# Kernel tuning notes

Measured on AMD Instinct MI355X. Metric: run time of the kernel, lower is better.

## Reference

```python
import jax, jax.numpy as jnp
import numpy as np

D = 1024
H = 16
HD = D // H  # 64


def setup_inputs() -> dict:
    key = jax.random.key(0)
    ks = jax.random.split(key, 12)
    B, S = 2, 2048
    inp = {
        "input_query": jax.random.normal(ks[0], (B, S, D), jnp.float32),
        "input_key": jax.random.normal(ks[1], (B, S, D), jnp.float32),
        "input_value": jax.random.normal(ks[2], (B, S, D), jnp.float32),
        "mask": jnp.ones((S, S), dtype=bool),  # ignored, as in original
        # per-head Q/K/V linears, stacked over heads: [H, D, HD]
        "Wq": jax.random.normal(ks[3], (H, D, HD), jnp.float32) / np.sqrt(D),
        "bq": jax.random.normal(ks[4], (H, HD), jnp.float32) * 0.01,
        "Wk": jax.random.normal(ks[5], (H, D, HD), jnp.float32) / np.sqrt(D),
        "bk": jax.random.normal(ks[6], (H, HD), jnp.float32) * 0.01,
        "Wv": jax.random.normal(ks[7], (H, D, HD), jnp.float32) / np.sqrt(D),
        "bv": jax.random.normal(ks[8], (H, HD), jnp.float32) * 0.01,
        "Wo": jax.random.normal(ks[9], (D, D), jnp.float32) / np.sqrt(D),
        "bo": jax.random.normal(ks[10], (D,), jnp.float32) * 0.01,
    }
    return inp


def reference(input_query, input_key, input_value, mask, Wq, bq, Wk, bk, Wv, bv, Wo, bo):
    B, S, _ = input_query.shape
    # batched per-head projections: [B,S,D] x [H,D,HD] -> [B,H,S,HD]
    q = jnp.einsum("bsd,hdk->bhsk", input_query, Wq) + bq[None, :, None, :]
    k = jnp.einsum("bsd,hdk->bhsk", input_key, Wk) + bk[None, :, None, :]
    v = jnp.einsum("bsd,hdk->bhsk", input_value, Wv) + bv[None, :, None, :]
    scale = 1.0 / np.sqrt(HD)
    scores = jnp.einsum("bhqk,bhsk->bhqs", q, k) * scale  # [B,H,S,S]
    causal = jnp.tril(jnp.ones((S, S), dtype=bool))
    scores = jnp.where(causal[None, None], scores, jnp.finfo(scores.dtype).min)
    p = jax.nn.softmax(scores, axis=-1)
    out = jnp.einsum("bhqs,bhsk->bhqk", p, v)  # [B,H,S,HD]
    # concat heads (matches torch.cat over head outputs on last dim)
    out = out.transpose(0, 2, 1, 3).reshape(B, S, D)
    return out @ Wo + bo
```

## Files before the change

kernel.cpp:

```cpp
#include <hip/hip_runtime.h>
#include <hip/hip_bf16.h>

typedef __bf16 bf16;
typedef bf16 bf16x8 __attribute__((ext_vector_type(8)));
typedef bf16 bf16x4 __attribute__((ext_vector_type(4)));
typedef float f32x4 __attribute__((ext_vector_type(4)));

#define B_  2
#define S_  2048
#define D_  1024
#define H_  16
#define HD_ 64
#define M_  4096
#define K_  1024
#define N_  1024

#if __has_builtin(__builtin_amdgcn_exp2f)
#define EXP2F(x) __builtin_amdgcn_exp2f(x)
#else
#define EXP2F(x) exp2f(x)
#endif

__device__ __forceinline__ void gld16(const bf16* g, bf16* l) {
    __builtin_amdgcn_global_load_lds(
        (const __attribute__((address_space(1))) unsigned int*)(g),
        (__attribute__((address_space(3))) unsigned int*)(l), 16, 0, 0);
}


__global__ void pack_x(const float* __restrict__ xq, const float* __restrict__ xk,
                       const float* __restrict__ xv, bf16* __restrict__ out) {
    int t = blockIdx.y;
    const float* src = (t == 0) ? xq : (t == 1) ? xk : xv;
    bf16* dst = out + (size_t)t * M_ * K_;
    int idx = (blockIdx.x * 256 + threadIdx.x) * 4;
    float4 v = *(const float4*)&src[idx];
    bf16x4 o = { (bf16)v.x, (bf16)v.y, (bf16)v.z, (bf16)v.w };
    *(bf16x4*)&dst[idx] = o;
}

__global__ void pack_w(const float* __restrict__ wq, const float* __restrict__ wk,
                       const float* __restrict__ wv, bf16* __restrict__ out) {
    int t = blockIdx.y;
    const float* src = (t == 0) ? wq : (t == 1) ? wk : wv;
    bf16* dst = out + (size_t)t * N_ * K_;
    int o = blockIdx.x * 256 + threadIdx.x;
    int n = o >> 10, k = o & 1023;
    dst[o] = (bf16)src[(n >> 6) * (D_ * HD_) + k * HD_ + (n & 63)];
}

__global__ void pack_wo(const float* __restrict__ wo, bf16* __restrict__ dst) {
    int o = blockIdx.x * 256 + threadIdx.x;
    int n = o >> 10, k = o & 1023;
    dst[o] = (bf16)wo[k * D_ + n];
}

__global__ __launch_bounds__(256) void gemm_qkv(
        const bf16* __restrict__ X, const bf16* __restrict__ Wt,
        const float* __restrict__ bq, const float* __restrict__ bk,
        const float* __restrict__ bv, bf16* __restrict__ QKV) {
    __shared__ __align__(16) bf16 As[128 * 32];
    __shared__ __align__(16) bf16 Bs[128 * 32];
    int t = blockIdx.z;
    const bf16* A = X + (size_t)t * M_ * K_;
    const bf16* W = Wt + (size_t)t * N_ * K_;
    const float* bias = (t == 0) ? bq : (t == 1) ? bk : bv;
    int m0 = blockIdx.x * 128, n0 = blockIdx.y * 128;
    int tid = threadIdx.x;
    int w = tid >> 6, l = tid & 63, lr = l & 15, lg = l >> 4;
    int wr = (w >> 1) * 64, wc = (w & 1) * 64;
    int srow = (l >> 2), scol = (l & 3) * 8;
    f32x4 acc[4][4] = {};
    for (int k0 = 0; k0 < K_; k0 += 32) {
        #pragma unroll
        for (int c = 0; c < 2; c++) {
            int chunk = w * 2 + c;
            gld16(&A[(size_t)(m0 + chunk * 16 + srow) * K_ + k0 + scol], &As[chunk * 512]);
            gld16(&W[(size_t)(n0 + chunk * 16 + srow) * K_ + k0 + scol], &Bs[chunk * 512]);
        }
        __syncthreads();
        bf16x8 af[4], bfr[4];
        #pragma unroll
        for (int mi = 0; mi < 4; mi++) af[mi] = *(const bf16x8*)&As[(wr + mi * 16 + lr) * 32 + lg * 8];
        #pragma unroll
        for (int ni = 0; ni < 4; ni++) bfr[ni] = *(const bf16x8*)&Bs[(wc + ni * 16 + lr) * 32 + lg * 8];
        #pragma unroll
        for (int mi = 0; mi < 4; mi++)
            #pragma unroll
            for (int ni = 0; ni < 4; ni++)
                acc[mi][ni] = __builtin_amdgcn_mfma_f32_16x16x32_bf16(af[mi], bfr[ni], acc[mi][ni], 0, 0, 0);
        __syncthreads();
    }
    float qscale = (t == 0) ? 0.125f * 1.4426950408889634f : 1.0f;
    #pragma unroll
    for (int mi = 0; mi < 4; mi++)
        #pragma unroll
        for (int ni = 0; ni < 4; ni++)
            #pragma unroll
            for (int i = 0; i < 4; i++) {
                int m = m0 + wr + mi * 16 + lg * 4 + i;
                int n = n0 + wc + ni * 16 + lr;
                float v = (acc[mi][ni][i] + bias[n]) * qscale;
                int b = m >> 11, s = m & 2047, h = n >> 6, hd = n & 63;
                QKV[((((size_t)t * B_ + b) * H_ + h) * S_ + s) * HD_ + hd] = (bf16)v;
            }
}

__global__ __launch_bounds__(256) void gemm_out(
        const bf16* __restrict__ A, const bf16* __restrict__ Wt,
        const float* __restrict__ bo, float* __restrict__ out) {
    __shared__ __align__(16) bf16 As[128 * 32];
    __shared__ __align__(16) bf16 Bs[128 * 32];
    int m0 = blockIdx.x * 128, n0 = blockIdx.y * 128;
    int tid = threadIdx.x;
    int w = tid >> 6, l = tid & 63, lr = l & 15, lg = l >> 4;
    int wr = (w >> 1) * 64, wc = (w & 1) * 64;
    int srow = (l >> 2), scol = (l & 3) * 8;
    f32x4 acc[4][4] = {};
    for (int k0 = 0; k0 < K_; k0 += 32) {
        #pragma unroll
        for (int c = 0; c < 2; c++) {
            int chunk = w * 2 + c;
            gld16(&A[(size_t)(m0 + chunk * 16 + srow) * K_ + k0 + scol], &As[chunk * 512]);
            gld16(&Wt[(size_t)(n0 + chunk * 16 + srow) * K_ + k0 + scol], &Bs[chunk * 512]);
        }
        __syncthreads();
        bf16x8 af[4], bfr[4];
        #pragma unroll
        for (int mi = 0; mi < 4; mi++) af[mi] = *(const bf16x8*)&As[(wr + mi * 16 + lr) * 32 + lg * 8];
        #pragma unroll
        for (int ni = 0; ni < 4; ni++) bfr[ni] = *(const bf16x8*)&Bs[(wc + ni * 16 + lr) * 32 + lg * 8];
        #pragma unroll
        for (int mi = 0; mi < 4; mi++)
            #pragma unroll
            for (int ni = 0; ni < 4; ni++)
                acc[mi][ni] = __builtin_amdgcn_mfma_f32_16x16x32_bf16(af[mi], bfr[ni], acc[mi][ni], 0, 0, 0);
        __syncthreads();
    }
    #pragma unroll
    for (int mi = 0; mi < 4; mi++)
        #pragma unroll
        for (int ni = 0; ni < 4; ni++)
            #pragma unroll
            for (int i = 0; i < 4; i++) {
                int m = m0 + wr + mi * 16 + lg * 4 + i;
                int n = n0 + wc + ni * 16 + lr;
                out[(size_t)m * N_ + n] = acc[mi][ni][i] + bo[n];
            }
}

__global__ __launch_bounds__(256) void transpose_v(const bf16* __restrict__ V,
                                                   bf16* __restrict__ VT) {
    __shared__ __align__(16) bf16 Ls[64][64];
    int s0 = blockIdx.x * 64, bh = blockIdx.y;
    const bf16* src = V + (size_t)bh * S_ * HD_;
    bf16* dst = VT + (size_t)bh * HD_ * S_;
    int tid = threadIdx.x;
    #pragma unroll
    for (int c = tid; c < 512; c += 256) {
        int row = c >> 3, cg = (c & 7) * 8;
        int cgp = cg ^ (((row >> 3) & 3) << 4);
        *(bf16x8*)&Ls[row][cgp] = *(const bf16x8*)&src[(size_t)(s0 + row) * 64 + cg];
    }
    __syncthreads();
    #pragma unroll
    for (int c = tid; c < 512; c += 256) {
        int hd = c >> 3, sg = (c & 7) * 8;
        bf16x8 v;
        #pragma unroll
        for (int e = 0; e < 8; e++) {
            int row = sg + e;
            v[e] = Ls[row][hd ^ (((row >> 3) & 3) << 4)];
        }
        *(bf16x8*)&dst[(size_t)hd * S_ + s0 + sg] = v;
    }
}

__global__ __launch_bounds__(512) void attn(const bf16* __restrict__ QKV,
                                            const bf16* __restrict__ VT,
                                            bf16* __restrict__ AO) {
    __shared__ __align__(16) bf16 Ks[2][64][72];
    __shared__ __align__(16) bf16 Vts[2][64][72];
    __shared__ __align__(16) bf16 Ps[8][16][72];
    int bh = blockIdx.y;
    int qt = (bh & 16) ? blockIdx.x : (15 - blockIdx.x);
    int q0 = qt * 128;
    const bf16* Qp = QKV + (size_t)bh * S_ * HD_;
    const bf16* Kp = QKV + (size_t)(32 + bh) * S_ * HD_;
    const bf16* VTp = VT + (size_t)bh * HD_ * S_;
    int tid = threadIdx.x, w = tid >> 6, l = tid & 63, lr = l & 15, lg = l >> 4;
    int srow = tid >> 3, scg = (tid & 7) * 8;

    bf16x8 aq[2];
    #pragma unroll
    for (int ks = 0; ks < 2; ks++)
        aq[ks] = *(const bf16x8*)&Qp[(size_t)(q0 + w * 16 + lr) * 64 + ks * 32 + lg * 8];

    f32x4 o[4] = {};
    float lsum[4] = {};
    int jmax = 2 * qt + 1;

    *(bf16x8*)&Ks[0][srow][scg]  = *(const bf16x8*)&Kp[(size_t)srow * 64 + scg];
    *(bf16x8*)&Vts[0][srow][scg] = *(const bf16x8*)&VTp[(size_t)srow * S_ + scg];
    __syncthreads();

    for (int j = 0; j <= jmax; ++j) {
        int cur = j & 1;
        if (j < jmax) {
            int nxt = cur ^ 1;
            *(bf16x8*)&Ks[nxt][srow][scg]  = *(const bf16x8*)&Kp[(size_t)((j + 1) * 64 + srow) * 64 + scg];
            *(bf16x8*)&Vts[nxt][srow][scg] = *(const bf16x8*)&VTp[(size_t)srow * S_ + (j + 1) * 64 + scg];
        }

        f32x4 sc[4] = {};
        __builtin_amdgcn_s_setprio(1);
        #pragma unroll
        for (int ks = 0; ks < 2; ks++)
            #pragma unroll
            for (int ni = 0; ni < 4; ni++) {
                bf16x8 bk_ = *(const bf16x8*)&Ks[cur][ni * 16 + lr][ks * 32 + lg * 8];
                sc[ni] = __builtin_amdgcn_mfma_f32_16x16x32_bf16(aq[ks], bk_, sc[ni], 0, 0, 0);
            }
        __builtin_amdgcn_s_setprio(0);

        bool diag = (j >= 2 * qt);
        int qrow = w * 16 + lg * 4;
        int kvb = j * 64 - q0;
        #pragma unroll
        for (int ni = 0; ni < 4; ni++)
            #pragma unroll
            for (int i = 0; i < 4; i++) {
                float s = sc[ni][i];
                if (diag && (kvb + ni * 16 + lr > qrow + i)) s = -30000.0f;
                float p = EXP2F(s);
                lsum[i] += p;
                Ps[w][lg * 4 + i][ni * 16 + lr] = (bf16)p;
            }

        __builtin_amdgcn_s_setprio(1);
        #pragma unroll
        for (int ks = 0; ks < 2; ks++) {
            bf16x8 ap = *(const bf16x8*)&Ps[w][lr][ks * 32 + lg * 8];
            #pragma unroll
            for (int nf = 0; nf < 4; nf++) {
                bf16x8 bv_ = *(const bf16x8*)&Vts[cur][nf * 16 + lr][ks * 32 + lg * 8];
                o[nf] = __builtin_amdgcn_mfma_f32_16x16x32_bf16(ap, bv_, o[nf], 0, 0, 0);
            }
        }
        __builtin_amdgcn_s_setprio(0);
        __syncthreads();
    }

    #pragma unroll
    for (int i = 0; i < 4; i++) {
        #pragma unroll
        for (int xm = 1; xm < 16; xm <<= 1) lsum[i] += __shfl_xor(lsum[i], xm);
    }

    int b = bh >> 4, h = bh & 15;
    #pragma unroll
    for (int i = 0; i < 4; i++) {
        float inv = 1.0f / lsum[i];
        #pragma unroll
        for (int nf = 0; nf < 4; nf++) {
            int m = b * S_ + q0 + w * 16 + lg * 4 + i;
            int d = h * 64 + nf * 16 + lr;
            AO[(size_t)m * D_ + d] = (bf16)(o[nf][i] * inv);
        }
    }
}

extern "C" void kernel_launch(void* const* d_in, const int* in_sizes, int n_in,
                              void* d_out, int out_size, void* d_ws, size_t ws_size,
                              hipStream_t stream) {
    const float* xq = (const float*)d_in[0];
    const float* xk = (const float*)d_in[1];
    const float* xv = (const float*)d_in[2];
    const float* wq = (const float*)d_in[4];
    const float* bq = (const float*)d_in[5];
    const float* wk = (const float*)d_in[6];
    const float* bk = (const float*)d_in[7];
    const float* wv = (const float*)d_in[8];
    const float* bv = (const float*)d_in[9];
    const float* wo = (const float*)d_in[10];
    const float* bo = (const float*)d_in[11];
    float* out = (float*)d_out;

    bf16* Xb  = (bf16*)d_ws;
    bf16* Wb  = Xb  + (size_t)3 * M_ * K_;
    bf16* WoT = Wb  + (size_t)3 * N_ * K_;
    bf16* QKV = WoT + (size_t)N_ * K_;
    bf16* AO  = QKV + (size_t)3 * M_ * K_;
    bf16* VT  = Xb;

    pack_x <<<dim3(M_ * K_ / 1024, 3), 256, 0, stream>>>(xq, xk, xv, Xb);
    pack_w <<<dim3(N_ * K_ / 256, 3), 256, 0, stream>>>(wq, wk, wv, Wb);
    pack_wo<<<dim3(N_ * K_ / 256), 256, 0, stream>>>(wo, WoT);
    gemm_qkv<<<dim3(M_ / 128, N_ / 128, 3), 256, 0, stream>>>(Xb, Wb, bq, bk, bv, QKV);
    transpose_v<<<dim3(S_ / 64, B_ * H_), 256, 0, stream>>>(QKV + (size_t)2 * M_ * K_, VT);
    attn    <<<dim3(S_ / 128, B_ * H_), 512, 0, stream>>>(QKV, VT, AO);
    gemm_out<<<dim3(M_ / 128, N_ / 128), 256, 0, stream>>>(AO, WoT, bo, out);
}
```

Baseline: 145.5 us.

## Load K/V fragments directly from global in attention, shrink q-tile, merge weight packing

The attention kernel stops staging K and V^T tiles through double-buffered shared memory with block-wide barriers. Each wave now loads its MFMA operand fragments straight from global memory, relying on cache for reuse. The q-tile per block shrinks from 128 to 64 rows with 256 threads, which doubles the block count and changes the causal load-balancing order. The Wo transpose-pack is also folded into pack_w, saving one launch. The trade is more global/L2 traffic per block in exchange for no barriers and less shared memory.

After: 318.9 us. 119% more time.

```diff
diff --git a/kernel.cpp b/kernel.cpp
--- a/kernel.cpp
+++ b/kernel.cpp
@@ -40,19 +40,18 @@
 }
 
 __global__ void pack_w(const float* __restrict__ wq, const float* __restrict__ wk,
-                       const float* __restrict__ wv, bf16* __restrict__ out) {
+                       const float* __restrict__ wv, const float* __restrict__ wo,
+                       bf16* __restrict__ out) {
     int t = blockIdx.y;
-    const float* src = (t == 0) ? wq : (t == 1) ? wk : wv;
     bf16* dst = out + (size_t)t * N_ * K_;
     int o = blockIdx.x * 256 + threadIdx.x;
     int n = o >> 10, k = o & 1023;
-    dst[o] = (bf16)src[(n >> 6) * (D_ * HD_) + k * HD_ + (n & 63)];
-}
-
-__global__ void pack_wo(const float* __restrict__ wo, bf16* __restrict__ dst) {
-    int o = blockIdx.x * 256 + threadIdx.x;
-    int n = o >> 10, k = o & 1023;
-    dst[o] = (bf16)wo[k * D_ + n];
+    if (t == 3) {
+        dst[o] = (bf16)wo[k * D_ + n];
+    } else {
+        const float* src = (t == 0) ? wq : (t == 1) ? wk : wv;
+        dst[o] = (bf16)src[(n >> 6) * (D_ * HD_) + k * HD_ + (n & 63)];
+    }
 }
 
 __global__ __launch_bounds__(256) void gemm_qkv(
@@ -176,62 +175,57 @@
     }
 }
 
-__global__ __launch_bounds__(512) void attn(const bf16* __restrict__ QKV,
+__global__ __launch_bounds__(256) void attn(const bf16* __restrict__ QKV,
                                             const bf16* __restrict__ VT,
                                             bf16* __restrict__ AO) {
-    __shared__ __align__(16) bf16 Ks[2][64][72];
-    __shared__ __align__(16) bf16 Vts[2][64][72];
-    __shared__ __align__(16) bf16 Ps[8][16][72];
+    __shared__ __align__(16) bf16 Ps[4][16][72];
     int bh = blockIdx.y;
-    int qt = (bh & 16) ? blockIdx.x : (15 - blockIdx.x);
-    int q0 = qt * 128;
+    int qt = (bh & 1) ? blockIdx.x : (31 - blockIdx.x);
     const bf16* Qp = QKV + (size_t)bh * S_ * HD_;
     const bf16* Kp = QKV + (size_t)(32 + bh) * S_ * HD_;
     const bf16* VTp = VT + (size_t)bh * HD_ * S_;
     int tid = threadIdx.x, w = tid >> 6, l = tid & 63, lr = l & 15, lg = l >> 4;
-    int srow = tid >> 3, scg = (tid & 7) * 8;
+    int qrow0 = qt * 64 + w * 16;
 
     bf16x8 aq[2];
     #pragma unroll
     for (int ks = 0; ks < 2; ks++)
-        aq[ks] = *(const bf16x8*)&Qp[(size_t)(q0 + w * 16 + lr) * 64 + ks * 32 + lg * 8];
+        aq[ks] = *(const bf16x8*)&Qp[(size_t)(qrow0 + lr) * 64 + ks * 32 + lg * 8];
 
     f32x4 o[4] = {};
     float lsum[4] = {};
-    int jmax = 2 * qt + 1;
-
-    *(bf16x8*)&Ks[0][srow][scg]  = *(const bf16x8*)&Kp[(size_t)srow * 64 + scg];
-    *(bf16x8*)&Vts[0][srow][scg] = *(const bf16x8*)&VTp[(size_t)srow * S_ + scg];
-    __syncthreads();
-
-    for (int j = 0; j <= jmax; ++j) {
-        int cur = j & 1;
-        if (j < jmax) {
-            int nxt = cur ^ 1;
-            *(bf16x8*)&Ks[nxt][srow][scg]  = *(const bf16x8*)&Kp[(size_t)((j + 1) * 64 + srow) * 64 + scg];
-            *(bf16x8*)&Vts[nxt][srow][scg] = *(const bf16x8*)&VTp[(size_t)srow * S_ + (j + 1) * 64 + scg];
-        }
+
+    for (int j = 0; j <= qt; ++j) {
+        bf16x8 bk[2][4];
+        #pragma unroll
+        for (int ks = 0; ks < 2; ks++)
+            #pragma unroll
+            for (int ni = 0; ni < 4; ni++)
+                bk[ks][ni] = *(const bf16x8*)&Kp[(size_t)(j * 64 + ni * 16 + lr) * 64 + ks * 32 + lg * 8];
 
         f32x4 sc[4] = {};
         __builtin_amdgcn_s_setprio(1);
         #pragma unroll
         for (int ks = 0; ks < 2; ks++)
             #pragma unroll
-            for (int ni = 0; ni < 4; ni++) {
-                bf16x8 bk_ = *(const bf16x8*)&Ks[cur][ni * 16 + lr][ks * 32 + lg * 8];
-                sc[ni] = __builtin_amdgcn_mfma_f32_16x16x32_bf16(aq[ks], bk_, sc[ni], 0, 0, 0);
-            }
+            for (int ni = 0; ni < 4; ni++)
+                sc[ni] = __builtin_amdgcn_mfma_f32_16x16x32_bf16(aq[ks], bk[ks][ni], sc[ni], 0, 0, 0);
         __builtin_amdgcn_s_setprio(0);
 
-        bool diag = (j >= 2 * qt);
-        int qrow = w * 16 + lg * 4;
-        int kvb = j * 64 - q0;
+        bf16x8 bv[2][4];
+        #pragma unroll
+        for (int ks = 0; ks < 2; ks++)
+            #pragma unroll
+            for (int nf = 0; nf < 4; nf++)
+                bv[ks][nf] = *(const bf16x8*)&VTp[(size_t)(nf * 16 + lr) * S_ + j * 64 + ks * 32 + lg * 8];
+
+        bool diag = (j == qt);
         #pragma unroll
         for (int ni = 0; ni < 4; ni++)
             #pragma unroll
             for (int i = 0; i < 4; i++) {
                 float s = sc[ni][i];
-                if (diag && (kvb + ni * 16 + lr > qrow + i)) s = -30000.0f;
+                if (diag && (ni * 16 + lr > w * 16 + lg * 4 + i)) s = -30000.0f;
                 float p = EXP2F(s);
                 lsum[i] += p;
                 Ps[w][lg * 4 + i][ni * 16 + lr] = (bf16)p;
@@ -242,13 +236,10 @@
         for (int ks = 0; ks < 2; ks++) {
             bf16x8 ap = *(const bf16x8*)&Ps[w][lr][ks * 32 + lg * 8];
             #pragma unroll
-            for (int nf = 0; nf < 4; nf++) {
-                bf16x8 bv_ = *(const bf16x8*)&Vts[cur][nf * 16 + lr][ks * 32 + lg * 8];
-                o[nf] = __builtin_amdgcn_mfma_f32_16x16x32_bf16(ap, bv_, o[nf], 0, 0, 0);
-            }
+            for (int nf = 0; nf < 4; nf++)
+                o[nf] = __builtin_amdgcn_mfma_f32_16x16x32_bf16(ap, bv[ks][nf], o[nf], 0, 0, 0);
         }
         __builtin_amdgcn_s_setprio(0);
-        __syncthreads();
     }
 
     #pragma unroll
@@ -263,7 +254,7 @@
         float inv = 1.0f / lsum[i];
         #pragma unroll
         for (int nf = 0; nf < 4; nf++) {
-            int m = b * S_ + q0 + w * 16 + lg * 4 + i;
+            int m = b * S_ + qrow0 + lg * 4 + i;
             int d = h * 64 + nf * 16 + lr;
             AO[(size_t)m * D_ + d] = (bf16)(o[nf][i] * inv);
         }
@@ -294,10 +285,9 @@
     bf16* VT  = Xb;
 
     pack_x <<<dim3(M_ * K_ / 1024, 3), 256, 0, stream>>>(xq, xk, xv, Xb);
-    pack_w <<<dim3(N_ * K_ / 256, 3), 256, 0, stream>>>(wq, wk, wv, Wb);
-    pack_wo<<<dim3(N_ * K_ / 256), 256, 0, stream>>>(wo, WoT);
+    pack_w <<<dim3(N_ * K_ / 256, 4), 256, 0, stream>>>(wq, wk, wv, wo, Wb);
     gemm_qkv<<<dim3(M_ / 128, N_ / 128, 3), 256, 0, stream>>>(Xb, Wb, bq, bk, bv, QKV);
     transpose_v<<<dim3(S_ / 64, B_ * H_), 256, 0, stream>>>(QKV + (size_t)2 * M_ * K_, VT);
-    attn    <<<dim3(S_ / 128, B_ * H_), 512, 0, stream>>>(QKV, VT, AO);
+    attn    <<<dim3(32, B_ * H_), 256, 0, stream>>>(QKV, VT, AO);
     gemm_out<<<dim3(M_ / 128, N_ / 128), 256, 0, stream>>>(AO, WoT, bo, out);
 }
```

## Double-buffer GEMM LDS tiles, register-stage attention prefetch, merge weight pack kernels

Applied to the files above, without the earlier changes.

Both GEMM kernels now keep two LDS buffers for the A and B tiles. The next K-slice is issued with async global-to-LDS loads before the MFMAs on the current slice run, which overlaps load latency with compute and removes one barrier per iteration. The attention kernel now loads the next K/V tile into registers early and writes it to shared memory only after the compute, hiding global latency behind the MFMAs. The Wo transpose-pack is folded into pack_w as a fourth grid slice, saving one kernel launch. The cost is twice the LDS per GEMM block, which may lower occupancy, and more live registers in attention.

Result: faster. 138.7 us (-4.7%).

```diff
diff --git a/kernel.cpp b/kernel.cpp
--- a/kernel.cpp
+++ b/kernel.cpp
@@ -40,27 +40,26 @@
 }
 
 __global__ void pack_w(const float* __restrict__ wq, const float* __restrict__ wk,
-                       const float* __restrict__ wv, bf16* __restrict__ out) {
+                       const float* __restrict__ wv, const float* __restrict__ wo,
+                       bf16* __restrict__ out) {
     int t = blockIdx.y;
-    const float* src = (t == 0) ? wq : (t == 1) ? wk : wv;
     bf16* dst = out + (size_t)t * N_ * K_;
     int o = blockIdx.x * 256 + threadIdx.x;
     int n = o >> 10, k = o & 1023;
-    dst[o] = (bf16)src[(n >> 6) * (D_ * HD_) + k * HD_ + (n & 63)];
-}
-
-__global__ void pack_wo(const float* __restrict__ wo, bf16* __restrict__ dst) {
-    int o = blockIdx.x * 256 + threadIdx.x;
-    int n = o >> 10, k = o & 1023;
-    dst[o] = (bf16)wo[k * D_ + n];
+    if (t == 3) {
+        dst[o] = (bf16)wo[k * D_ + n];
+    } else {
+        const float* src = (t == 0) ? wq : (t == 1) ? wk : wv;
+        dst[o] = (bf16)src[(n >> 6) * (D_ * HD_) + k * HD_ + (n & 63)];
+    }
 }
 
 __global__ __launch_bounds__(256) void gemm_qkv(
         const bf16* __restrict__ X, const bf16* __restrict__ Wt,
         const float* __restrict__ bq, const float* __restrict__ bk,
         const float* __restrict__ bv, bf16* __restrict__ QKV) {
-    __shared__ __align__(16) bf16 As[128 * 32];
-    __shared__ __align__(16) bf16 Bs[128 * 32];
+    __shared__ __align__(16) bf16 As[2][128 * 32];
+    __shared__ __align__(16) bf16 Bs[2][128 * 32];
     int t = blockIdx.z;
     const bf16* A = X + (size_t)t * M_ * K_;
     const bf16* W = Wt + (size_t)t * N_ * K_;
@@ -71,19 +70,28 @@
     int wr = (w >> 1) * 64, wc = (w & 1) * 64;
     int srow = (l >> 2), scol = (l & 3) * 8;
     f32x4 acc[4][4] = {};
+    #pragma unroll
+    for (int c = 0; c < 2; c++) {
+        int chunk = w * 2 + c;
+        gld16(&A[(size_t)(m0 + chunk * 16 + srow) * K_ + scol], &As[0][chunk * 512]);
+        gld16(&W[(size_t)(n0 + chunk * 16 + srow) * K_ + scol], &Bs[0][chunk * 512]);
+    }
+    __syncthreads();
     for (int k0 = 0; k0 < K_; k0 += 32) {
-        #pragma unroll
-        for (int c = 0; c < 2; c++) {
-            int chunk = w * 2 + c;
-            gld16(&A[(size_t)(m0 + chunk * 16 + srow) * K_ + k0 + scol], &As[chunk * 512]);
-            gld16(&W[(size_t)(n0 + chunk * 16 + srow) * K_ + k0 + scol], &Bs[chunk * 512]);
-        }
-        __syncthreads();
+        int cur = (k0 >> 5) & 1, nxt = cur ^ 1;
+        if (k0 + 32 < K_) {
+            #pragma unroll
+            for (int c = 0; c < 2; c++) {
+                int chunk = w * 2 + c;
+                gld16(&A[(size_t)(m0 + chunk * 16 + srow) * K_ + k0 + 32 + scol], &As[nxt][chunk * 512]);
+                gld16(&W[(size_t)(n0 + chunk * 16 + srow) * K_ + k0 + 32 + scol], &Bs[nxt][chunk * 512]);
+            }
+        }
         bf16x8 af[4], bfr[4];
         #pragma unroll
-        for (int mi = 0; mi < 4; mi++) af[mi] = *(const bf16x8*)&As[(wr + mi * 16 + lr) * 32 + lg * 8];
-        #pragma unroll
-        for (int ni = 0; ni < 4; ni++) bfr[ni] = *(const bf16x8*)&Bs[(wc + ni * 16 + lr) * 32 + lg * 8];
+        for (int mi = 0; mi < 4; mi++) af[mi] = *(const bf16x8*)&As[cur][(wr + mi * 16 + lr) * 32 + lg * 8];
+        #pragma unroll
+        for (int ni = 0; ni < 4; ni++) bfr[ni] = *(const bf16x8*)&Bs[cur][(wc + ni * 16 + lr) * 32 + lg * 8];
         #pragma unroll
         for (int mi = 0; mi < 4; mi++)
             #pragma unroll
@@ -109,27 +117,36 @@
 __global__ __launch_bounds__(256) void gemm_out(
         const bf16* __restrict__ A, const bf16* __restrict__ Wt,
         const float* __restrict__ bo, float* __restrict__ out) {
-    __shared__ __align__(16) bf16 As[128 * 32];
-    __shared__ __align__(16) bf16 Bs[128 * 32];
+    __shared__ __align__(16) bf16 As[2][128 * 32];
+    __shared__ __align__(16) bf16 Bs[2][128 * 32];
     int m0 = blockIdx.x * 128, n0 = blockIdx.y * 128;
     int tid = threadIdx.x;
     int w = tid >> 6, l = tid & 63, lr = l & 15, lg = l >> 4;
     int wr = (w >> 1) * 64, wc = (w & 1) * 64;
     int srow = (l >> 2), scol = (l & 3) * 8;
     f32x4 acc[4][4] = {};
+    #pragma unroll
+    for (int c = 0; c < 2; c++) {
+        int chunk = w * 2 + c;
+        gld16(&A[(size_t)(m0 + chunk * 16 + srow) * K_ + scol], &As[0][chunk * 512]);
+        gld16(&Wt[(size_t)(n0 + chunk * 16 + srow) * K_ + scol], &Bs[0][chunk * 512]);
+    }
+    __syncthreads();
     for (int k0 = 0; k0 < K_; k0 += 32) {
-        #pragma unroll
-        for (int c = 0; c < 2; c++) {
-            int chunk = w * 2 + c;
-            gld16(&A[(size_t)(m0 + chunk * 16 + srow) * K_ + k0 + scol], &As[chunk * 512]);
-            gld16(&Wt[(size_t)(n0 + chunk * 16 + srow) * K_ + k0 + scol], &Bs[chunk * 512]);
-        }
-        __syncthreads();
+        int cur = (k0 >> 5) & 1, nxt = cur ^ 1;
+        if (k0 + 32 < K_) {
+            #pragma unroll
+            for (int c = 0; c < 2; c++) {
+                int chunk = w * 2 + c;
+                gld16(&A[(size_t)(m0 + chunk * 16 + srow) * K_ + k0 + 32 + scol], &As[nxt][chunk * 512]);
+                gld16(&Wt[(size_t)(n0 + chunk * 16 + srow) * K_ + k0 + 32 + scol], &Bs[nxt][chunk * 512]);
+            }
+        }
         bf16x8 af[4], bfr[4];
         #pragma unroll
-        for (int mi = 0; mi < 4; mi++) af[mi] = *(const bf16x8*)&As[(wr + mi * 16 + lr) * 32 + lg * 8];
-        #pragma unroll
-        for (int ni = 0; ni < 4; ni++) bfr[ni] = *(const bf16x8*)&Bs[(wc + ni * 16 + lr) * 32 + lg * 8];
+        for (int mi = 0; mi < 4; mi++) af[mi] = *(const bf16x8*)&As[cur][(wr + mi * 16 + lr) * 32 + lg * 8];
+        #pragma unroll
+        for (int ni = 0; ni < 4; ni++) bfr[ni] = *(const bf16x8*)&Bs[cur][(wc + ni * 16 + lr) * 32 + lg * 8];
         #pragma unroll
         for (int mi = 0; mi < 4; mi++)
             #pragma unroll
@@ -206,10 +223,11 @@
 
     for (int j = 0; j <= jmax; ++j) {
         int cur = j & 1;
-        if (j < jmax) {
-            int nxt = cur ^ 1;
-            *(bf16x8*)&Ks[nxt][srow][scg]  = *(const bf16x8*)&Kp[(size_t)((j + 1) * 64 + srow) * 64 + scg];
-            *(bf16x8*)&Vts[nxt][srow][scg] = *(const bf16x8*)&VTp[(size_t)srow * S_ + (j + 1) * 64 + scg];
+        bool pf = (j < jmax);
+        bf16x8 kreg, vreg;
+        if (pf) {
+            kreg = *(const bf16x8*)&Kp[(size_t)((j + 1) * 64 + srow) * 64 + scg];
+            vreg = *(const bf16x8*)&VTp[(size_t)srow * S_ + (j + 1) * 64 + scg];
         }
 
         f32x4 sc[4] = {};
@@ -248,6 +266,11 @@
             }
         }
         __builtin_amdgcn_s_setprio(0);
+
+        if (pf) {
+            *(bf16x8*)&Ks[cur ^ 1][srow][scg]  = kreg;
+            *(bf16x8*)&Vts[cur ^ 1][srow][scg] = vreg;
+        }
         __syncthreads();
     }
 
@@ -294,8 +317,7 @@
     bf16* VT  = Xb;
 
     pack_x <<<dim3(M_ * K_ / 1024, 3), 256, 0, stream>>>(xq, xk, xv, Xb);
-    pack_w <<<dim3(N_ * K_ / 256, 3), 256, 0, stream>>>(wq, wk, wv, Wb);
-    pack_wo<<<dim3(N_ * K_ / 256), 256, 0, stream>>>(wo, WoT);
+    pack_w <<<dim3(N_ * K_ / 256, 4), 256, 0, stream>>>(wq, wk, wv, wo, Wb);
     gemm_qkv<<<dim3(M_ / 128, N_ / 128, 3), 256, 0, stream>>>(Xb, Wb, bq, bk, bv, QKV);
     transpose_v<<<dim3(S_ / 64, B_ * H_), 256, 0, stream>>>(QKV + (size_t)2 * M_ * K_, VT);
     attn    <<<dim3(S_ / 128, B_ * H_), 512, 0, stream>>>(QKV, VT, AO);
```
